# Kernel tuning notes

Hardware: AMD Instinct MI355X
Metric: run time of the kernel (lower is better)

Reference implementation:

```python
import jax, jax.numpy as jnp
import numpy as np

EPS = 1e-5
SEQ = 64

def ln(x, g, b):
    m = jnp.mean(x, axis=-1, keepdims=True)
    v = jnp.var(x, axis=-1, keepdims=True)
    return (x - m) / jnp.sqrt(v + EPS) * g + b

def gelu(x):
    return jax.nn.gelu(x, approximate=False)  # torch nn.GELU default = exact erf

def setup_inputs() -> dict:
    key = jax.random.key(0)
    ks = jax.random.split(key, 24)
    B, D = 512, 128
    DSGU = 4 * D          # 512
    DATTN = DSGU // 2     # 256
    DEXP = 4 * D          # 512 (tiny-attn expanded dim)
    TF = SEQ * D          # 8192
    H = int(1.1 * TF)     # 9011
    w = lambda k, s: jax.random.normal(k, s, dtype=jnp.float32) * 0.02
    return {
        "x": jax.random.normal(ks[0], (B, SEQ, D), dtype=jnp.float32),
        # TinyAttentionBlock
        "qkv_ln_g": jnp.ones((D,), jnp.float32), "qkv_ln_b": jnp.zeros((D,), jnp.float32),
        "qkv_w": w(ks[1], (D, 3 * DEXP)), "qkv_b": jnp.zeros((3 * DEXP,), jnp.float32),
        "attn_proj_w": w(ks[2], (DEXP, DATTN)), "attn_proj_b": jnp.zeros((DATTN,), jnp.float32),
        "attn_ln_g": jnp.ones((DATTN,), jnp.float32), "attn_ln_b": jnp.zeros((DATTN,), jnp.float32),
        "rel_bias": w(ks[3], (2 * SEQ - 1,)),
        "scale": jnp.asarray(1.0 / np.sqrt(D), jnp.float32),
        # SGU proj_in / proj_spatial / proj_out
        "pin_ln_g": jnp.ones((D,), jnp.float32), "pin_ln_b": jnp.zeros((D,), jnp.float32),
        "pin_w": w(ks[4], (D, DSGU)), "pin_b": jnp.zeros((DSGU,), jnp.float32),
        "sp_ln_g": jnp.ones((SEQ,), jnp.float32), "sp_ln_b": jnp.zeros((SEQ,), jnp.float32),
        "sp_w": w(ks[5], (SEQ, SEQ)), "sp_b": jnp.ones((SEQ,), jnp.float32),  # bias init 1.0 per source
        "pout_ln_g": jnp.ones((DATTN,), jnp.float32), "pout_ln_b": jnp.zeros((DATTN,), jnp.float32),
        "pout_w": w(ks[6], (DATTN, D)), "pout_b": jnp.zeros((D,), jnp.float32),
        # ResidualBlock MLP
        "mlp_ln_g": jnp.ones((TF,), jnp.float32), "mlp_ln_b": jnp.zeros((TF,), jnp.float32),
        "mlp_w1": w(ks[7], (TF, H)), "mlp_b1": jnp.zeros((H,), jnp.float32),
        "mlp_w2": w(ks[8], (H, TF)), "mlp_b2": jnp.zeros((TF,), jnp.float32),
    }

def reference(x, qkv_ln_g, qkv_ln_b, qkv_w, qkv_b, attn_proj_w, attn_proj_b,
              attn_ln_g, attn_ln_b, rel_bias, scale,
              pin_ln_g, pin_ln_b, pin_w, pin_b, sp_ln_g, sp_ln_b, sp_w, sp_b,
              pout_ln_g, pout_ln_b, pout_w, pout_b,
              mlp_ln_g, mlp_ln_b, mlp_w1, mlp_b1, mlp_w2, mlp_b2):
    B = x.shape[0]
    # --- TinyAttentionBlock ---
    h = ln(x, qkv_ln_g, qkv_ln_b) @ qkv_w + qkv_b          # [B,64,3*512]
    q, k, v = jnp.split(h, 3, axis=-1)                      # each [B,64,512]
    idx = jnp.arange(SEQ)
    rel = idx[None, :] - idx[:, None] + (SEQ - 1)           # [64,64] in [0,126]
    bias = rel_bias[rel]                                    # [64,64]
    attn = jnp.einsum('bnd,bmd->bnm', q, k) + bias
    attn = jax.nn.softmax(attn, axis=-1) * scale            # post-softmax scale (as in source)
    av = jnp.einsum('bnm,bmd->bnd', attn, v)                # [B,64,512]
    a = ln(av @ attn_proj_w + attn_proj_b, attn_ln_g, attn_ln_b)  # [B,64,256]
    # --- SpatialGatingUnit ---
    h2 = gelu(ln(x, pin_ln_g, pin_ln_b) @ pin_w + pin_b)    # [B,64,512]
    u, vv = jnp.split(h2, 2, axis=-1)                        # [B,64,256] each
    vt = jnp.swapaxes(vv, 1, 2)                              # [B,256,64]
    vt = gelu(ln(vt, sp_ln_g, sp_ln_b) @ sp_w + sp_b)        # spatial proj over seq dim
    vv = jnp.swapaxes(vt, 1, 2)                              # [B,64,256]
    out = u * (vv + a)
    out = ln(out, pout_ln_g, pout_ln_b) @ pout_w + pout_b    # [B,64,128]
    x = x + out
    # --- ResidualBlock MLP on flattened board ---
    xf = x.reshape(B, -1)                                    # [B,8192]
    h3 = gelu(ln(xf, mlp_ln_g, mlp_ln_b) @ mlp_w1 + mlp_b1)  # [B,9011]
    xf = xf + (h3 @ mlp_w2 + mlp_b2)
    return xf.reshape(B, SEQ, -1)
```

## Files before the change

### kernel.cpp

```cpp
#include <hip/hip_runtime.h>
#include <hip/hip_bf16.h>
#include <math.h>

typedef float f32x4 __attribute__((ext_vector_type(4)));
typedef float f32x2 __attribute__((ext_vector_type(2)));
typedef short s16x8 __attribute__((ext_vector_type(8)));
typedef short s16x4 __attribute__((ext_vector_type(4)));
typedef int   i32x4 __attribute__((ext_vector_type(4)));

__device__ __forceinline__ short f2bf(float f) {
  __hip_bfloat16 h = __float2bfloat16(f);
  return __builtin_bit_cast(short, h);
}
__device__ __forceinline__ float bf2f(short s) {
  __hip_bfloat16 h = __builtin_bit_cast(__hip_bfloat16, s);
  return __bfloat162float(h);
}
__device__ __forceinline__ float gelu_f(float x) {
  return 0.5f * x * (1.f + erff(x * 0.70710678118654752440f));
}
__device__ __forceinline__ float waveSum(float v) {
  #pragma unroll
  for (int d = 32; d; d >>= 1) v += __shfl_xor(v, d);
  return v;
}
__device__ __forceinline__ void softBarrier() {
  asm volatile("s_waitcnt lgkmcnt(0)" ::: "memory");
  __builtin_amdgcn_s_barrier();
  asm volatile("" ::: "memory");
}

__global__ __launch_bounds__(256) void ln_dual_k(
    const float* __restrict__ x,
    const float* __restrict__ qg, const float* __restrict__ qb,
    const float* __restrict__ pg, const float* __restrict__ pb,
    short* __restrict__ lnq, short* __restrict__ lnp)
{
  int w = threadIdx.x >> 6, lane = threadIdx.x & 63;
  size_t row = (size_t)blockIdx.x * 4 + w;
  f32x2 v = reinterpret_cast<const f32x2*>(x + row * 128)[lane];
  float s  = v[0] + v[1];
  float sq = v[0]*v[0] + v[1]*v[1];
  s = waveSum(s); sq = waveSum(sq);
  float m = s * (1.f/128.f);
  float rstd = rsqrtf(sq * (1.f/128.f) - m*m + 1e-5f);
  int c = lane * 2;
  float a0 = (v[0]-m)*rstd, a1 = (v[1]-m)*rstd;
  unsigned q0 = (unsigned short)f2bf(a0*qg[c] + qb[c]);
  unsigned q1 = (unsigned short)f2bf(a1*qg[c+1] + qb[c+1]);
  unsigned p0 = (unsigned short)f2bf(a0*pg[c] + pb[c]);
  unsigned p1 = (unsigned short)f2bf(a1*pg[c+1] + pb[c+1]);
  ((unsigned*)lnq)[row*64 + lane] = q0 | (q1 << 16);
  ((unsigned*)lnp)[row*64 + lane] = p0 | (p1 << 16);
}

__global__ __launch_bounds__(256) void ln256_k(
    const float* __restrict__ in,
    const float* __restrict__ g, const float* __restrict__ bb,
    float* __restrict__ out)
{
  int w = threadIdx.x >> 6, lane = threadIdx.x & 63;
  size_t row = (size_t)blockIdx.x * 4 + w;
  f32x4 v = reinterpret_cast<const f32x4*>(in + row * 256)[lane];
  float s  = v[0]+v[1]+v[2]+v[3];
  float sq = v[0]*v[0]+v[1]*v[1]+v[2]*v[2]+v[3]*v[3];
  s = waveSum(s); sq = waveSum(sq);
  float m = s * (1.f/256.f);
  float rstd = rsqrtf(sq * (1.f/256.f) - m*m + 1e-5f);
  f32x4 g4 = reinterpret_cast<const f32x4*>(g)[lane];
  f32x4 b4 = reinterpret_cast<const f32x4*>(bb)[lane];
  f32x4 o;
  #pragma unroll
  for (int k = 0; k < 4; ++k) o[k] = (v[k]-m)*rstd*g4[k] + b4[k];
  reinterpret_cast<f32x4*>(out + row * 256)[lane] = o;
}

__global__ __launch_bounds__(256) void ln8192_k(
    const float* __restrict__ x1,
    const float* __restrict__ g, const float* __restrict__ bb,
    short* __restrict__ lnxp)
{
  __shared__ float red[8];
  int t = threadIdx.x, w = t >> 6, lane = t & 63;
  int b = blockIdx.x;
  const f32x4* xr = reinterpret_cast<const f32x4*>(x1 + (size_t)b * 8192);
  f32x4 vals[8];
  float s = 0.f, sq = 0.f;
  #pragma unroll
  for (int i = 0; i < 8; ++i) {
    f32x4 v = xr[t + i*256];
    vals[i] = v;
    s  += v[0]+v[1]+v[2]+v[3];
    sq += v[0]*v[0]+v[1]*v[1]+v[2]*v[2]+v[3]*v[3];
  }
  s = waveSum(s); sq = waveSum(sq);
  if (lane == 0) { red[w] = s; red[4+w] = sq; }
  __syncthreads();
  s  = red[0]+red[1]+red[2]+red[3];
  sq = red[4]+red[5]+red[6]+red[7];
  float m = s * (1.f/8192.f);
  float rstd = rsqrtf(sq * (1.f/8192.f) - m*m + 1e-5f);
  #pragma unroll
  for (int i = 0; i < 8; ++i) {
    int idx = (t + i*256) * 4;
    f32x4 g4 = reinterpret_cast<const f32x4*>(g)[t + i*256];
    f32x4 b4 = reinterpret_cast<const f32x4*>(bb)[t + i*256];
    s16x4 o;
    #pragma unroll
    for (int k = 0; k < 4; ++k) o[k] = f2bf((vals[i][k]-m)*rstd*g4[k] + b4[k]);
    size_t paddr = ((size_t)(idx >> 6) * 512 + b) * 64 + (idx & 63);
    *reinterpret_cast<s16x4*>(&lnxp[paddr]) = o;
  }
}

template<int BM, int BN, int WM, int WN, int EPI>
__global__ __launch_bounds__(256) void gemm_k(
    const short* __restrict__ A, const float* __restrict__ Bw,
    const float* __restrict__ bias, const float* __restrict__ res,
    void* __restrict__ O0, void* __restrict__ O1,
    int M, int N, int K, int Nreal, int Kreal)
{
  constexpr int BK = 64;
  __shared__ __align__(16) short As[BM][BK + 8];
  __shared__ __align__(16) short Bs[BN][BK + 8];
  const int t = threadIdx.x;
  const int lane = t & 63;
  const int w = t >> 6;
  const int wm = w / WN, wn = w % WN;
  const int ln15 = lane & 15, hi = lane >> 4;
  const int m0 = blockIdx.y * BM;
  const int n0 = blockIdx.x * BN;

  f32x4 acc[4][4] = {};

  for (int k0 = 0; k0 < K; k0 += BK) {
    #pragma unroll
    for (int i = 0; i < (BM*BK)/(256*8); ++i) {
      int e = (i*256 + t) * 8;
      int r = e / BK, c = e % BK;
      *reinterpret_cast<i32x4*>(&As[r][c]) =
          *reinterpret_cast<const i32x4*>(&A[(size_t)(m0 + r) * K + k0 + c]);
    }
    #pragma unroll
    for (int i = 0; i < (BK*BN)/256; ++i) {
      int idx = i*256 + t;
      int n = idx % BN, k = idx / BN;
      int gk = k0 + k, gn = n0 + n;
      float v = (gk < Kreal && gn < Nreal) ? Bw[(size_t)gk * Nreal + gn] : 0.f;
      Bs[n][k] = f2bf(v);
    }
    __syncthreads();
    #pragma unroll
    for (int kk = 0; kk < BK; kk += 32) {
      s16x8 af[4], bfr[4];
      #pragma unroll
      for (int fm = 0; fm < 4; ++fm)
        af[fm] = *reinterpret_cast<const s16x8*>(&As[wm*64 + fm*16 + ln15][kk + hi*8]);
      #pragma unroll
      for (int fn = 0; fn < 4; ++fn)
        bfr[fn] = *reinterpret_cast<const s16x8*>(&Bs[wn*64 + fn*16 + ln15][kk + hi*8]);
      #pragma unroll
      for (int fm = 0; fm < 4; ++fm)
        #pragma unroll
        for (int fn = 0; fn < 4; ++fn)
          acc[fm][fn] = __builtin_amdgcn_mfma_f32_16x16x32_bf16(
              af[fm], bfr[fn], acc[fm][fn], 0, 0, 0);
    }
    __syncthreads();
  }

  #pragma unroll
  for (int fm = 0; fm < 4; ++fm) {
    #pragma unroll
    for (int fn = 0; fn < 4; ++fn) {
      #pragma unroll
      for (int j = 0; j < 4; ++j) {
        int row = m0 + wm*64 + fm*16 + hi*4 + j;
        int col = n0 + wn*64 + fn*16 + ln15;
        float v = acc[fm][fn][j];
        if constexpr (EPI == 0) {
          v += bias[col];
          ((short*)O0)[(size_t)row * N + col] = f2bf(v);
        } else if constexpr (EPI == 1) {
          v += bias[col];
          ((float*)O0)[(size_t)row * N + col] = v;
        } else if constexpr (EPI == 2) {
          v = gelu_f(v + bias[col]);
          if (col < 256) ((float*)O0)[(size_t)row * 256 + col] = v;
          else ((short*)O1)[(size_t)row * 256 + (col - 256)] = f2bf(v);
        } else {
          v += bias[col] + res[(size_t)row * N + col];
          ((float*)O0)[(size_t)row * N + col] = v;
        }
      }
    }
  }
}

__global__ __launch_bounds__(512, 2) void gemm_splitk9(
    const short* __restrict__ Ap, const float* __restrict__ Bw,
    float* __restrict__ part,
    int N, int K, int Kreal, int ldb, int kchunk, int ntiles)
{
  __shared__ __align__(16) short Bs[2][128 * 64];
  const int t = threadIdx.x, lane = t & 63, w = t >> 6;
  const int ln15 = lane & 15, hi = lane >> 4;
  const int nt = blockIdx.x % ntiles, z = blockIdx.x / ntiles;
  const int n0 = nt * 128;
  const int kbeg = z * kchunk;
  const int kend = (kbeg + kchunk < K) ? (kbeg + kchunk) : K;
  const int nsteps = (kend - kbeg) >> 6;

  const int bn = t & 127;
  const int bg0 = (t >> 7) * 2;
  const bool bok = (n0 + bn) < ldb;
  const int bsw = bn & 7;

  float br[16];
  auto loadB = [&](int k0) {
    const float* bp = Bw + (size_t)(k0 + bg0 * 8) * ldb + n0 + bn;
    #pragma unroll
    for (int m = 0; m < 16; ++m) {
      int gk = k0 + bg0 * 8 + m;
      br[m] = (bok && gk < Kreal) ? bp[(size_t)m * ldb] : 0.f;
    }
  };
  auto writeB = [&](int buf) {
    s16x8 v0, v1;
    #pragma unroll
    for (int m = 0; m < 8; ++m) { v0[m] = f2bf(br[m]); v1[m] = f2bf(br[8 + m]); }
    short* dst = &Bs[buf][bn * 64];
    *reinterpret_cast<s16x8*>(dst + ((bg0    ) ^ bsw) * 8) = v0;
    *reinterpret_cast<s16x8*>(dst + ((bg0 + 1) ^ bsw) * 8) = v1;
  };

  f32x4 acc[4][8] = {};

  loadB(kbeg);
  writeB(0);
  if (nsteps > 1) loadB(kbeg + 64);
  softBarrier();

  for (int s = 0; s < nsteps; ++s) {
    const int k0 = kbeg + s * 64;
    const short* atile = Ap + (size_t)(k0 >> 6) * 512 * 64;
    s16x8 af[8];
    #pragma unroll
    for (int kk = 0; kk < 2; ++kk)
      #pragma unroll
      for (int fm = 0; fm < 4; ++fm) {
        int row = w * 64 + fm * 16 + ln15;
        af[kk * 4 + fm] = *reinterpret_cast<const s16x8*>(
            &atile[row * 64 + (kk * 4 + hi) * 8]);
      }
    if (s + 1 < nsteps) writeB((s + 1) & 1);
    if (s + 2 < nsteps) loadB(kbeg + (s + 2) * 64);

    const short* bsrc = &Bs[s & 1][0];
    #pragma unroll
    for (int kk = 0; kk < 2; ++kk) {
      const int g = kk * 4 + hi;
      #pragma unroll
      for (int fn = 0; fn < 8; ++fn) {
        int row = fn * 16 + ln15;
        s16x8 bv = *reinterpret_cast<const s16x8*>(
            &bsrc[row * 64 + ((g ^ (row & 7)) * 8)]);
        #pragma unroll
        for (int fm = 0; fm < 4; ++fm)
          acc[fm][fn] = __builtin_amdgcn_mfma_f32_16x16x32_bf16(
              af[kk * 4 + fm], bv, acc[fm][fn], 0, 0, 0);
      }
    }
    softBarrier();
  }

  #pragma unroll
  for (int fm = 0; fm < 4; ++fm)
    #pragma unroll
    for (int fn = 0; fn < 8; ++fn)
      #pragma unroll
      for (int j = 0; j < 4; ++j) {
        int row = w * 64 + fm * 16 + hi * 4 + j;
        int col = n0 + fn * 16 + ln15;
        part[((size_t)z * 512 + row) * N + col] = acc[fm][fn][j];
      }
}

__global__ __launch_bounds__(256) void reduce_mlp1_k(
    const float* __restrict__ part, const float* __restrict__ bias,
    short* __restrict__ h3p, int N, int Nreal, int M, int ks)
{
  int col4 = (blockIdx.x * 256 + threadIdx.x) * 4;
  int row = blockIdx.y;
  if (col4 >= N) return;
  size_t base = (size_t)row * N + col4;
  size_t stride = (size_t)M * N;
  f32x4 s = *reinterpret_cast<const f32x4*>(part + base);
  for (int k = 1; k < ks; ++k)
    s += *reinterpret_cast<const f32x4*>(part + base + (size_t)k * stride);
  s16x4 o;
  #pragma unroll
  for (int j = 0; j < 4; ++j) {
    int c = col4 + j;
    float v = 0.f;
    if (c < Nreal) v = gelu_f(s[j] + bias[c]);
    o[j] = f2bf(v);
  }
  size_t paddr = ((size_t)(col4 >> 6) * 512 + row) * 64 + (col4 & 63);
  *reinterpret_cast<s16x4*>(&h3p[paddr]) = o;
}

__global__ __launch_bounds__(256) void reduce_mlp2_k(
    const float* __restrict__ part, const float* __restrict__ bias,
    const float* __restrict__ x1, float* __restrict__ out, int N, int M, int ks)
{
  int col4 = (blockIdx.x * 256 + threadIdx.x) * 4;
  int row = blockIdx.y;
  size_t base = (size_t)row * N + col4;
  size_t stride = (size_t)M * N;
  f32x4 s = *reinterpret_cast<const f32x4*>(part + base);
  for (int k = 1; k < ks; ++k)
    s += *reinterpret_cast<const f32x4*>(part + base + (size_t)k * stride);
  f32x4 b4 = *reinterpret_cast<const f32x4*>(bias + col4);
  f32x4 r4 = *reinterpret_cast<const f32x4*>(x1 + base);
  #pragma unroll
  for (int j = 0; j < 4; ++j) s[j] += b4[j] + r4[j];
  *reinterpret_cast<f32x4*>(out + base) = s;
}

__global__ __launch_bounds__(256) void attn_k(
    const short* __restrict__ qkv, const float* __restrict__ relb,
    const float* __restrict__ scale_p, short* __restrict__ av)
{
  __shared__ __align__(16) short qlds[64][136];
  __shared__ __align__(16) short klds[64][136];
  __shared__ __align__(16) short plds[64][72];
  __shared__ __align__(16) short vlds[128][72];
  __shared__ float rb[127];
  int t = threadIdx.x, lane = t & 63, w = t >> 6;
  int ln15 = lane & 15, hi = lane >> 4;
  int b = blockIdx.x;
  if (t < 127) rb[t] = relb[t];

  f32x4 sacc[4] = {};
  for (int kc = 0; kc < 4; ++kc) {
    #pragma unroll
    for (int i = 0; i < 4; ++i) {
      int e = (i*256 + t) * 8;
      int r = e >> 7, c = e & 127;
      size_t base = (size_t)(b*64 + r) * 1536 + kc*128 + c;
      *reinterpret_cast<i32x4*>(&qlds[r][c]) = *reinterpret_cast<const i32x4*>(&qkv[base]);
      *reinterpret_cast<i32x4*>(&klds[r][c]) = *reinterpret_cast<const i32x4*>(&qkv[base + 512]);
    }
    __syncthreads();
    #pragma unroll
    for (int kk = 0; kk < 128; kk += 32) {
      s16x8 aq = *reinterpret_cast<const s16x8*>(&qlds[16*w + ln15][kk + hi*8]);
      #pragma unroll
      for (int fn = 0; fn < 4; ++fn) {
        s16x8 bk = *reinterpret_cast<const s16x8*>(&klds[fn*16 + ln15][kk + hi*8]);
        sacc[fn] = __builtin_amdgcn_mfma_f32_16x16x32_bf16(aq, bk, sacc[fn], 0, 0, 0);
      }
    }
    __syncthreads();
  }

  float scale = scale_p[0];
  #pragma unroll
  for (int j = 0; j < 4; ++j) {
    int row = 16*w + hi*4 + j;
    float pv[4];
    float mx = -1e30f;
    #pragma unroll
    for (int fn = 0; fn < 4; ++fn) {
      int col = fn*16 + ln15;
      pv[fn] = sacc[fn][j] + rb[col - row + 63];
      mx = fmaxf(mx, pv[fn]);
    }
    #pragma unroll
    for (int d = 1; d < 16; d <<= 1) mx = fmaxf(mx, __shfl_xor(mx, d));
    float sum = 0.f;
    #pragma unroll
    for (int fn = 0; fn < 4; ++fn) { pv[fn] = __expf(pv[fn] - mx); sum += pv[fn]; }
    #pragma unroll
    for (int d = 1; d < 16; d <<= 1) sum += __shfl_xor(sum, d);
    float inv = scale / sum;
    #pragma unroll
    for (int fn = 0; fn < 4; ++fn) plds[row][fn*16 + ln15] = f2bf(pv[fn] * inv);
  }
  __syncthreads();

  for (int cc = 0; cc < 4; ++cc) {
    #pragma unroll
    for (int i = 0; i < 8; ++i) {
      int idx = i*256 + t;
      int s = idx >> 5, c4 = (idx & 31) * 4;
      s16x4 vw = *reinterpret_cast<const s16x4*>(
          &qkv[(size_t)(b*64 + s) * 1536 + 1024 + cc*128 + c4]);
      vlds[c4+0][s] = vw[0]; vlds[c4+1][s] = vw[1];
      vlds[c4+2][s] = vw[2]; vlds[c4+3][s] = vw[3];
    }
    __syncthreads();
    f32x4 pacc[8] = {};
    #pragma unroll
    for (int kk = 0; kk < 64; kk += 32) {
      s16x8 ap = *reinterpret_cast<const s16x8*>(&plds[16*w + ln15][kk + hi*8]);
      #pragma unroll
      for (int fn = 0; fn < 8; ++fn) {
        s16x8 bv = *reinterpret_cast<const s16x8*>(&vlds[fn*16 + ln15][kk + hi*8]);
        pacc[fn] = __builtin_amdgcn_mfma_f32_16x16x32_bf16(ap, bv, pacc[fn], 0, 0, 0);
      }
    }
    #pragma unroll
    for (int fn = 0; fn < 8; ++fn)
      #pragma unroll
      for (int j = 0; j < 4; ++j) {
        int row = b*64 + 16*w + hi*4 + j;
        int col = cc*128 + fn*16 + ln15;
        av[(size_t)row * 512 + col] = f2bf(pacc[fn][j]);
      }
    __syncthreads();
  }
}

__global__ __launch_bounds__(256) void gate_k(
    const float* __restrict__ u, const short* __restrict__ vbf,
    const float* __restrict__ a,
    const float* __restrict__ spg_g, const float* __restrict__ spg_b,
    const float* __restrict__ spw, const float* __restrict__ spb,
    const float* __restrict__ pog, const float* __restrict__ pob,
    short* __restrict__ outn)
{
  __shared__ __align__(16) short nvb[256][72];
  __shared__ __align__(16) short spwT[64][72];
  __shared__ float s_spg[64], s_spbl[64], s_spb[64];
  __shared__ float s_pog[256], s_pob[256];
  int t = threadIdx.x, lane = t & 63, w = t >> 6;
  int ln15 = lane & 15, hi = lane >> 4;
  int b = blockIdx.x;

  if (t < 64) { s_spg[t] = spg_g[t]; s_spbl[t] = spg_b[t]; s_spb[t] = spb[t]; }
  s_pog[t] = pog[t]; s_pob[t] = pob[t];
  #pragma unroll
  for (int i = 0; i < 16; ++i) {
    int idx = i*256 + t;
    int sr = idx >> 6, tc = idx & 63;
    spwT[tc][sr] = f2bf(spw[idx]);
  }

  float vvv[64];
  {
    int c = t;
    float s = 0.f, sq = 0.f;
    #pragma unroll
    for (int si = 0; si < 64; ++si) {
      float f = bf2f(vbf[(size_t)(b*64 + si) * 256 + c]);
      vvv[si] = f; s += f; sq += f*f;
    }
    float m = s * (1.f/64.f);
    float rstd = rsqrtf(sq * (1.f/64.f) - m*m + 1e-5f);
    __syncthreads();
    #pragma unroll
    for (int si = 0; si < 64; ++si)
      nvb[c][si] = f2bf((vvv[si]-m)*rstd*s_spg[si] + s_spbl[si]);
  }
  __syncthreads();

  f32x4 yacc[4][4] = {};
  #pragma unroll
  for (int kk = 0; kk < 64; kk += 32) {
    s16x8 af[4], bfr[4];
    #pragma unroll
    for (int fm = 0; fm < 4; ++fm)
      af[fm] = *reinterpret_cast<const s16x8*>(&nvb[64*w + fm*16 + ln15][kk + hi*8]);
    #pragma unroll
    for (int fn = 0; fn < 4; ++fn)
      bfr[fn] = *reinterpret_cast<const s16x8*>(&spwT[fn*16 + ln15][kk + hi*8]);
    #pragma unroll
    for (int fm = 0; fm < 4; ++fm)
      #pragma unroll
      for (int fn = 0; fn < 4; ++fn)
        yacc[fm][fn] = __builtin_amdgcn_mfma_f32_16x16x32_bf16(
            af[fm], bfr[fn], yacc[fm][fn], 0, 0, 0);
  }
  __syncthreads();

  short (*outl)[264] = reinterpret_cast<short(*)[264]>(&nvb[0][0]);
  #pragma unroll
  for (int fm = 0; fm < 4; ++fm) {
    #pragma unroll
    for (int fn = 0; fn < 4; ++fn) {
      int crow = 64*w + fm*16 + hi*4;
      int tcol = fn*16 + ln15;
      f32x4 u4 = *reinterpret_cast<const f32x4*>(&u[(size_t)(b*64 + tcol)*256 + crow]);
      f32x4 a4 = *reinterpret_cast<const f32x4*>(&a[(size_t)(b*64 + tcol)*256 + crow]);
      #pragma unroll
      for (int j = 0; j < 4; ++j) {
        float g = gelu_f(yacc[fm][fn][j] + s_spb[tcol]);
        float o = u4[j] * (g + a4[j]);
        outl[tcol][crow + j] = f2bf(o);
      }
    }
  }
  __syncthreads();

  #pragma unroll
  for (int ri = 0; ri < 16; ++ri) {
    int trow = w*16 + ri;
    int c = lane * 4;
    s16x4 raw = *reinterpret_cast<const s16x4*>(&outl[trow][c]);
    float f0 = bf2f(raw[0]), f1 = bf2f(raw[1]), f2 = bf2f(raw[2]), f3 = bf2f(raw[3]);
    float s  = f0+f1+f2+f3;
    float sq = f0*f0+f1*f1+f2*f2+f3*f3;
    s = waveSum(s); sq = waveSum(sq);
    float m = s * (1.f/256.f);
    float rstd = rsqrtf(sq * (1.f/256.f) - m*m + 1e-5f);
    s16x4 o;
    o[0] = f2bf((f0-m)*rstd*s_pog[c+0] + s_pob[c+0]);
    o[1] = f2bf((f1-m)*rstd*s_pog[c+1] + s_pob[c+1]);
    o[2] = f2bf((f2-m)*rstd*s_pog[c+2] + s_pob[c+2]);
    o[3] = f2bf((f3-m)*rstd*s_pog[c+3] + s_pob[c+3]);
    *reinterpret_cast<s16x4*>(&outn[(size_t)(b*64 + trow)*256 + c]) = o;
  }
}

extern "C" void kernel_launch(void* const* d_in, const int* in_sizes, int n_in,
                              void* d_out, int out_size, void* d_ws, size_t ws_size,
                              hipStream_t stream)
{
  const float* x          = (const float*)d_in[0];
  const float* qkv_ln_g   = (const float*)d_in[1];
  const float* qkv_ln_b   = (const float*)d_in[2];
  const float* qkv_w      = (const float*)d_in[3];
  const float* qkv_b      = (const float*)d_in[4];
  const float* attn_pw    = (const float*)d_in[5];
  const float* attn_pb    = (const float*)d_in[6];
  const float* attn_ln_g  = (const float*)d_in[7];
  const float* attn_ln_b  = (const float*)d_in[8];
  const float* rel_bias   = (const float*)d_in[9];
  const float* scale      = (const float*)d_in[10];
  const float* pin_ln_g   = (const float*)d_in[11];
  const float* pin_ln_b   = (const float*)d_in[12];
  const float* pin_w      = (const float*)d_in[13];
  const float* pin_b      = (const float*)d_in[14];
  const float* sp_ln_g    = (const float*)d_in[15];
  const float* sp_ln_b    = (const float*)d_in[16];
  const float* sp_w       = (const float*)d_in[17];
  const float* sp_b       = (const float*)d_in[18];
  const float* pout_ln_g  = (const float*)d_in[19];
  const float* pout_ln_b  = (const float*)d_in[20];
  const float* pout_w     = (const float*)d_in[21];
  const float* pout_b     = (const float*)d_in[22];
  const float* mlp_ln_g   = (const float*)d_in[23];
  const float* mlp_ln_b   = (const float*)d_in[24];
  const float* mlp_w1     = (const float*)d_in[25];
  const float* mlp_b1     = (const float*)d_in[26];
  const float* mlp_w2     = (const float*)d_in[27];
  const float* mlp_b2     = (const float*)d_in[28];

  char* ws = (char*)d_ws;
  short* lnq  = (short*)(ws + 0);
  short* lnp  = (short*)(ws + 8388608);
  short* qkvb = (short*)(ws + 16777216);
  short* avb  = (short*)(ws + 117440512);
  float* projb= (float*)(ws + 16777216);
  float* ab   = (float*)(ws + 50331648);
  float* ub   = (float*)(ws + 83886080);
  short* vbfb = (short*)(ws + 117440512);
  short* outnb= (short*)(ws + 134217728);
  float* x1b  = (float*)(ws + 0);
  short* lnxp = (short*)(ws + 150994944);
  short* h3p  = (short*)(ws + 159383552);
  float* partb= (float*)(ws + 16777216);

  ln_dual_k<<<8192, 256, 0, stream>>>(x, qkv_ln_g, qkv_ln_b, pin_ln_g, pin_ln_b, lnq, lnp);
  gemm_k<128,128,2,2,0><<<dim3(12,256), 256, 0, stream>>>(
      lnq, qkv_w, qkv_b, nullptr, qkvb, nullptr, 32768, 1536, 128, 1536, 128);
  attn_k<<<512, 256, 0, stream>>>(qkvb, rel_bias, scale, avb);
  gemm_k<128,128,2,2,1><<<dim3(2,256), 256, 0, stream>>>(
      avb, attn_pw, attn_pb, nullptr, projb, nullptr, 32768, 256, 512, 256, 512);
  ln256_k<<<8192, 256, 0, stream>>>(projb, attn_ln_g, attn_ln_b, ab);
  gemm_k<128,128,2,2,2><<<dim3(4,256), 256, 0, stream>>>(
      lnp, pin_w, pin_b, nullptr, ub, vbfb, 32768, 512, 128, 512, 128);
  gate_k<<<512, 256, 0, stream>>>(ub, vbfb, ab, sp_ln_g, sp_ln_b, sp_w, sp_b,
                                  pout_ln_g, pout_ln_b, outnb);
  gemm_k<128,128,2,2,3><<<dim3(1,256), 256, 0, stream>>>(
      outnb, pout_w, pout_b, x, x1b, nullptr, 32768, 128, 256, 128, 256);
  ln8192_k<<<512, 256, 0, stream>>>(x1b, mlp_ln_g, mlp_ln_b, lnxp);

  gemm_splitk9<<<213, 512, 0, stream>>>(
      lnxp, mlp_w1, partb, 9088, 8192, 8192,
      9011, 2752, 71);
  reduce_mlp1_k<<<dim3(9, 512), 256, 0, stream>>>(partb, mlp_b1, h3p, 9088, 9011, 512, 3);

  gemm_splitk9<<<256, 512, 0, stream>>>(
      h3p, mlp_w2, partb, 8192, 9088, 9011,
      8192, 2304, 64);
  reduce_mlp2_k<<<dim3(8, 512), 256, 0, stream>>>(partb, mlp_b2, x1b, (float*)d_out, 8192, 512, 4);
}
```

Measured before the change: 769.2 us.

## Fuse LayerNorm, QKV projection, attention, output projection and LN into one kernel

Replaces five launches (dual LN, QKV GEMM, attention, attn-proj GEMM, LN256) with a single per-batch kernel. Each block keeps LN output, Q/K/V chunks, the softmax probabilities and the attention output in LDS, so the large qkv, av and proj intermediates never go to global memory. In exchange, every block re-reads and converts the fp32 qkv_w and attn_proj_w weights into transposed bf16 LDS tiles. It also uses about 159 KB of LDS, which allows only one 4-wave block per CU and leaves little latency hiding.

```diff
diff --git a/kernel.cpp b/kernel.cpp
--- a/kernel.cpp
+++ b/kernel.cpp
@@ -30,86 +30,225 @@
   asm volatile("" ::: "memory");
 }
 
-__global__ __launch_bounds__(256) void ln_dual_k(
+__global__ __launch_bounds__(256) void fused_attn_k(
     const float* __restrict__ x,
-    const float* __restrict__ qg, const float* __restrict__ qb,
-    const float* __restrict__ pg, const float* __restrict__ pb,
-    short* __restrict__ lnq, short* __restrict__ lnp)
-{
-  int w = threadIdx.x >> 6, lane = threadIdx.x & 63;
-  size_t row = (size_t)blockIdx.x * 4 + w;
-  f32x2 v = reinterpret_cast<const f32x2*>(x + row * 128)[lane];
-  float s  = v[0] + v[1];
-  float sq = v[0]*v[0] + v[1]*v[1];
-  s = waveSum(s); sq = waveSum(sq);
-  float m = s * (1.f/128.f);
-  float rstd = rsqrtf(sq * (1.f/128.f) - m*m + 1e-5f);
-  int c = lane * 2;
-  float a0 = (v[0]-m)*rstd, a1 = (v[1]-m)*rstd;
-  unsigned q0 = (unsigned short)f2bf(a0*qg[c] + qb[c]);
-  unsigned q1 = (unsigned short)f2bf(a1*qg[c+1] + qb[c+1]);
-  unsigned p0 = (unsigned short)f2bf(a0*pg[c] + pb[c]);
-  unsigned p1 = (unsigned short)f2bf(a1*pg[c+1] + pb[c+1]);
-  ((unsigned*)lnq)[row*64 + lane] = q0 | (q1 << 16);
-  ((unsigned*)lnp)[row*64 + lane] = p0 | (p1 << 16);
-}
-
-__global__ __launch_bounds__(256) void ln256_k(
-    const float* __restrict__ in,
-    const float* __restrict__ g, const float* __restrict__ bb,
-    float* __restrict__ out)
-{
-  int w = threadIdx.x >> 6, lane = threadIdx.x & 63;
-  size_t row = (size_t)blockIdx.x * 4 + w;
-  f32x4 v = reinterpret_cast<const f32x4*>(in + row * 256)[lane];
-  float s  = v[0]+v[1]+v[2]+v[3];
-  float sq = v[0]*v[0]+v[1]*v[1]+v[2]*v[2]+v[3]*v[3];
-  s = waveSum(s); sq = waveSum(sq);
-  float m = s * (1.f/256.f);
-  float rstd = rsqrtf(sq * (1.f/256.f) - m*m + 1e-5f);
-  f32x4 g4 = reinterpret_cast<const f32x4*>(g)[lane];
-  f32x4 b4 = reinterpret_cast<const f32x4*>(bb)[lane];
-  f32x4 o;
-  #pragma unroll
-  for (int k = 0; k < 4; ++k) o[k] = (v[k]-m)*rstd*g4[k] + b4[k];
-  reinterpret_cast<f32x4*>(out + row * 256)[lane] = o;
-}
-
-__global__ __launch_bounds__(256) void ln8192_k(
-    const float* __restrict__ x1,
-    const float* __restrict__ g, const float* __restrict__ bb,
-    short* __restrict__ lnxp)
-{
-  __shared__ float red[8];
-  int t = threadIdx.x, w = t >> 6, lane = t & 63;
-  int b = blockIdx.x;
-  const f32x4* xr = reinterpret_cast<const f32x4*>(x1 + (size_t)b * 8192);
-  f32x4 vals[8];
-  float s = 0.f, sq = 0.f;
-  #pragma unroll
-  for (int i = 0; i < 8; ++i) {
-    f32x4 v = xr[t + i*256];
-    vals[i] = v;
-    s  += v[0]+v[1]+v[2]+v[3];
-    sq += v[0]*v[0]+v[1]*v[1]+v[2]*v[2]+v[3]*v[3];
-  }
-  s = waveSum(s); sq = waveSum(sq);
-  if (lane == 0) { red[w] = s; red[4+w] = sq; }
+    const float* __restrict__ qln_g, const float* __restrict__ qln_b,
+    const float* __restrict__ pln_g, const float* __restrict__ pln_b,
+    const float* __restrict__ qkv_w, const float* __restrict__ qkv_b,
+    const float* __restrict__ attn_pw, const float* __restrict__ attn_pb,
+    const float* __restrict__ aln_g, const float* __restrict__ aln_b,
+    const float* __restrict__ relb, const float* __restrict__ scale_p,
+    short* __restrict__ lnp, float* __restrict__ ab)
+{
+  __shared__ __align__(16) char arena[159232];
+  short (*lnq)[136]  = reinterpret_cast<short(*)[136]>(arena + 0);
+  short (*plds)[72]  = reinterpret_cast<short(*)[72]>(arena + 17408);
+  short (*vlds)[72]  = reinterpret_cast<short(*)[72]>(arena + 26624);
+  short (*avl)[136]  = reinterpret_cast<short(*)[136]>(arena + 26624);
+  short (*qlds)[136] = reinterpret_cast<short(*)[136]>(arena + 45056);
+  short (*klds)[136] = reinterpret_cast<short(*)[136]>(arena + 62464);
+  short (*pwT)[136]  = reinterpret_cast<short(*)[136]>(arena + 45056);
+  short (*wT)[136]   = reinterpret_cast<short(*)[136]>(arena + 114688);
+  float* rb    = reinterpret_cast<float*>(arena + 149504);
+  float* s_apb = reinterpret_cast<float*>(arena + 150016);
+  float* s_ag  = reinterpret_cast<float*>(arena + 151040);
+  float* s_ab2 = reinterpret_cast<float*>(arena + 152064);
+  float* sqb   = reinterpret_cast<float*>(arena + 153088);
+
+  const int t = threadIdx.x, lane = t & 63, w = t >> 6;
+  const int ln15 = lane & 15, hi = lane >> 4;
+  const int b = blockIdx.x;
+
+  if (t < 127) rb[t] = relb[t];
+  s_apb[t] = attn_pb[t]; s_ag[t] = aln_g[t]; s_ab2[t] = aln_b[t];
+  #pragma unroll
+  for (int i = 0; i < 6; ++i) sqb[i*256 + t] = qkv_b[i*256 + t];
+
+  {
+    int c = lane * 2;
+    float qg0 = qln_g[c], qg1 = qln_g[c+1], qb0 = qln_b[c], qb1 = qln_b[c+1];
+    float pg0 = pln_g[c], pg1 = pln_g[c+1], pb0 = pln_b[c], pb1 = pln_b[c+1];
+    for (int i = 0; i < 16; ++i) {
+      int r = w * 16 + i;
+      f32x2 v = *reinterpret_cast<const f32x2*>(&x[((size_t)b*64 + r)*128 + c]);
+      float s = v[0] + v[1], sq = v[0]*v[0] + v[1]*v[1];
+      s = waveSum(s); sq = waveSum(sq);
+      float m = s * (1.f/128.f);
+      float rstd = rsqrtf(sq*(1.f/128.f) - m*m + 1e-5f);
+      float a0 = (v[0]-m)*rstd, a1 = (v[1]-m)*rstd;
+      unsigned q0 = (unsigned short)f2bf(a0*qg0 + qb0);
+      unsigned q1 = (unsigned short)f2bf(a1*qg1 + qb1);
+      *reinterpret_cast<unsigned*>(&lnq[r][c]) = q0 | (q1 << 16);
+      unsigned p0 = (unsigned short)f2bf(a0*pg0 + pb0);
+      unsigned p1 = (unsigned short)f2bf(a1*pg1 + pb1);
+      ((unsigned*)lnp)[((size_t)b*64 + r)*64 + lane] = p0 | (p1 << 16);
+    }
+  }
   __syncthreads();
-  s  = red[0]+red[1]+red[2]+red[3];
-  sq = red[4]+red[5]+red[6]+red[7];
-  float m = s * (1.f/8192.f);
-  float rstd = rsqrtf(sq * (1.f/8192.f) - m*m + 1e-5f);
-  #pragma unroll
-  for (int i = 0; i < 8; ++i) {
-    int idx = (t + i*256) * 4;
-    f32x4 g4 = reinterpret_cast<const f32x4*>(g)[t + i*256];
-    f32x4 b4 = reinterpret_cast<const f32x4*>(bb)[t + i*256];
-    s16x4 o;
-    #pragma unroll
-    for (int k = 0; k < 4; ++k) o[k] = f2bf((vals[i][k]-m)*rstd*g4[k] + b4[k]);
-    size_t paddr = ((size_t)(idx >> 6) * 512 + b) * 64 + (idx & 63);
-    *reinterpret_cast<s16x4*>(&lnxp[paddr]) = o;
+
+  auto stageW = [&](int coff) {
+    #pragma unroll
+    for (int i = 0; i < 16; ++i) {
+      int e = i*256 + t;
+      int k = e >> 5, c4 = (e & 31) * 4;
+      f32x4 v = *reinterpret_cast<const f32x4*>(&qkv_w[(size_t)k*1536 + coff + c4]);
+      wT[c4+0][k] = f2bf(v[0]); wT[c4+1][k] = f2bf(v[1]);
+      wT[c4+2][k] = f2bf(v[2]); wT[c4+3][k] = f2bf(v[3]);
+    }
+  };
+  auto gemm8 = [&](f32x4 (&acc)[8]) {
+    #pragma unroll
+    for (int kk = 0; kk < 4; ++kk) {
+      s16x8 af = *reinterpret_cast<const s16x8*>(&lnq[w*16 + ln15][kk*32 + hi*8]);
+      #pragma unroll
+      for (int fn = 0; fn < 8; ++fn) {
+        s16x8 bf = *reinterpret_cast<const s16x8*>(&wT[fn*16 + ln15][kk*32 + hi*8]);
+        acc[fn] = __builtin_amdgcn_mfma_f32_16x16x32_bf16(af, bf, acc[fn], 0, 0, 0);
+      }
+    }
+  };
+
+  f32x4 sacc[4] = {};
+  for (int kc = 0; kc < 4; ++kc) {
+    __syncthreads();
+    stageW(kc * 128);
+    __syncthreads();
+    {
+      f32x4 qa[8] = {};
+      gemm8(qa);
+      #pragma unroll
+      for (int fn = 0; fn < 8; ++fn) {
+        float bias = sqb[kc*128 + fn*16 + ln15];
+        #pragma unroll
+        for (int j = 0; j < 4; ++j)
+          qlds[w*16 + hi*4 + j][fn*16 + ln15] = f2bf(qa[fn][j] + bias);
+      }
+    }
+    __syncthreads();
+    stageW(512 + kc * 128);
+    __syncthreads();
+    {
+      f32x4 ka[8] = {};
+      gemm8(ka);
+      #pragma unroll
+      for (int fn = 0; fn < 8; ++fn) {
+        float bias = sqb[512 + kc*128 + fn*16 + ln15];
+        #pragma unroll
+        for (int j = 0; j < 4; ++j)
+          klds[w*16 + hi*4 + j][fn*16 + ln15] = f2bf(ka[fn][j] + bias);
+      }
+    }
+    __syncthreads();
+    #pragma unroll
+    for (int kk = 0; kk < 4; ++kk) {
+      s16x8 aq = *reinterpret_cast<const s16x8*>(&qlds[16*w + ln15][kk*32 + hi*8]);
+      #pragma unroll
+      for (int fn = 0; fn < 4; ++fn) {
+        s16x8 bk = *reinterpret_cast<const s16x8*>(&klds[fn*16 + ln15][kk*32 + hi*8]);
+        sacc[fn] = __builtin_amdgcn_mfma_f32_16x16x32_bf16(aq, bk, sacc[fn], 0, 0, 0);
+      }
+    }
+  }
+
+  {
+    float scale = scale_p[0];
+    #pragma unroll
+    for (int j = 0; j < 4; ++j) {
+      int row = 16*w + hi*4 + j;
+      float pv[4];
+      float mx = -1e30f;
+      #pragma unroll
+      for (int fn = 0; fn < 4; ++fn) {
+        int col = fn*16 + ln15;
+        pv[fn] = sacc[fn][j] + rb[col - row + 63];
+        mx = fmaxf(mx, pv[fn]);
+      }
+      #pragma unroll
+      for (int d = 1; d < 16; d <<= 1) mx = fmaxf(mx, __shfl_xor(mx, d));
+      float sum = 0.f;
+      #pragma unroll
+      for (int fn = 0; fn < 4; ++fn) { pv[fn] = __expf(pv[fn] - mx); sum += pv[fn]; }
+      #pragma unroll
+      for (int d = 1; d < 16; d <<= 1) sum += __shfl_xor(sum, d);
+      float inv = scale / sum;
+      #pragma unroll
+      for (int fn = 0; fn < 4; ++fn) plds[row][fn*16 + ln15] = f2bf(pv[fn] * inv);
+    }
+  }
+  __syncthreads();
+
+  f32x4 pracc[16] = {};
+  for (int cc = 0; cc < 4; ++cc) {
+    __syncthreads();
+    stageW(1024 + cc * 128);
+    #pragma unroll
+    for (int i = 0; i < 32; ++i) {
+      int e = i*256 + t;
+      int k = e >> 6, c4 = (e & 63) * 4;
+      f32x4 v = *reinterpret_cast<const f32x4*>(&attn_pw[(size_t)(cc*128 + k)*256 + c4]);
+      pwT[c4+0][k] = f2bf(v[0]); pwT[c4+1][k] = f2bf(v[1]);
+      pwT[c4+2][k] = f2bf(v[2]); pwT[c4+3][k] = f2bf(v[3]);
+    }
+    __syncthreads();
+    {
+      f32x4 va[8] = {};
+      gemm8(va);
+      #pragma unroll
+      for (int fn = 0; fn < 8; ++fn) {
+        float bias = sqb[1024 + cc*128 + fn*16 + ln15];
+        #pragma unroll
+        for (int j = 0; j < 4; ++j)
+          vlds[fn*16 + ln15][w*16 + hi*4 + j] = f2bf(va[fn][j] + bias);
+      }
+    }
+    __syncthreads();
+    f32x4 pacc[8] = {};
+    #pragma unroll
+    for (int kk = 0; kk < 2; ++kk) {
+      s16x8 ap = *reinterpret_cast<const s16x8*>(&plds[16*w + ln15][kk*32 + hi*8]);
+      #pragma unroll
+      for (int fn = 0; fn < 8; ++fn) {
+        s16x8 bv = *reinterpret_cast<const s16x8*>(&vlds[fn*16 + ln15][kk*32 + hi*8]);
+        pacc[fn] = __builtin_amdgcn_mfma_f32_16x16x32_bf16(ap, bv, pacc[fn], 0, 0, 0);
+      }
+    }
+    __syncthreads();
+    #pragma unroll
+    for (int fn = 0; fn < 8; ++fn)
+      #pragma unroll
+      for (int j = 0; j < 4; ++j)
+        avl[w*16 + hi*4 + j][fn*16 + ln15] = f2bf(pacc[fn][j]);
+    __syncthreads();
+    #pragma unroll
+    for (int kk = 0; kk < 4; ++kk) {
+      s16x8 aa = *reinterpret_cast<const s16x8*>(&avl[16*w + ln15][kk*32 + hi*8]);
+      #pragma unroll
+      for (int fn = 0; fn < 16; ++fn) {
+        s16x8 pb = *reinterpret_cast<const s16x8*>(&pwT[fn*16 + ln15][kk*32 + hi*8]);
+        pracc[fn] = __builtin_amdgcn_mfma_f32_16x16x32_bf16(aa, pb, pracc[fn], 0, 0, 0);
+      }
+    }
+  }
+
+  #pragma unroll
+  for (int j = 0; j < 4; ++j) {
+    int row = 16*w + hi*4 + j;
+    float vv[16];
+    float s = 0.f, sq = 0.f;
+    #pragma unroll
+    for (int fn = 0; fn < 16; ++fn) {
+      vv[fn] = pracc[fn][j] + s_apb[fn*16 + ln15];
+      s += vv[fn]; sq += vv[fn]*vv[fn];
+    }
+    #pragma unroll
+    for (int d = 1; d < 16; d <<= 1) { s += __shfl_xor(s, d); sq += __shfl_xor(sq, d); }
+    float m = s * (1.f/256.f);
+    float rstd = rsqrtf(sq*(1.f/256.f) - m*m + 1e-5f);
+    #pragma unroll
+    for (int fn = 0; fn < 16; ++fn) {
+      int col = fn*16 + ln15;
+      ab[((size_t)b*64 + row)*256 + col] = (vv[fn]-m)*rstd*s_ag[col] + s_ab2[col];
+    }
   }
 }
 
@@ -178,13 +317,7 @@
         int row = m0 + wm*64 + fm*16 + hi*4 + j;
         int col = n0 + wn*64 + fn*16 + ln15;
         float v = acc[fm][fn][j];
-        if constexpr (EPI == 0) {
-          v += bias[col];
-          ((short*)O0)[(size_t)row * N + col] = f2bf(v);
-        } else if constexpr (EPI == 1) {
-          v += bias[col];
-          ((float*)O0)[(size_t)row * N + col] = v;
-        } else if constexpr (EPI == 2) {
+        if constexpr (EPI == 2) {
           v = gelu_f(v + bias[col]);
           if (col < 256) ((float*)O0)[(size_t)row * 256 + col] = v;
           else ((short*)O1)[(size_t)row * 256 + (col - 256)] = f2bf(v);
@@ -194,6 +327,44 @@
         }
       }
     }
+  }
+}
+
+__global__ __launch_bounds__(256) void ln8192_k(
+    const float* __restrict__ x1,
+    const float* __restrict__ g, const float* __restrict__ bb,
+    short* __restrict__ lnxp)
+{
+  __shared__ float red[8];
+  int t = threadIdx.x, w = t >> 6, lane = t & 63;
+  int b = blockIdx.x;
+  const f32x4* xr = reinterpret_cast<const f32x4*>(x1 + (size_t)b * 8192);
+  f32x4 vals[8];
+  float s = 0.f, sq = 0.f;
+  #pragma unroll
+  for (int i = 0; i < 8; ++i) {
+    f32x4 v = xr[t + i*256];
+    vals[i] = v;
+    s  += v[0]+v[1]+v[2]+v[3];
+    sq += v[0]*v[0]+v[1]*v[1]+v[2]*v[2]+v[3]*v[3];
+  }
+  s = waveSum(s); sq = waveSum(sq);
+  if (lane == 0) { red[w] = s; red[4+w] = sq; }
+  __syncthreads();
+  s  = red[0]+red[1]+red[2]+red[3];
+  sq = red[4]+red[5]+red[6]+red[7];
+  float m = s * (1.f/8192.f);
+  float rstd = rsqrtf(sq * (1.f/8192.f) - m*m + 1e-5f);
+  #pragma unroll
+  for (int i = 0; i < 8; ++i) {
+    int idx = (t + i*256) * 4;
+    f32x4 g4 = reinterpret_cast<const f32x4*>(g)[t + i*256];
+    f32x4 b4 = reinterpret_cast<const f32x4*>(bb)[t + i*256];
+    s16x4 o;
+    #pragma unroll
+    for (int k = 0; k < 4; ++k) o[k] = f2bf((vals[i][k]-m)*rstd*g4[k] + b4[k]);
+    size_t paddr = ((size_t)(idx >> 6) * 512 + b) * 64 + (idx & 63);
+    *reinterpret_cast<s16x4*>(&lnxp[paddr]) = o;
   }
 }
 
@@ -326,101 +497,6 @@
   #pragma unroll
   for (int j = 0; j < 4; ++j) s[j] += b4[j] + r4[j];
   *reinterpret_cast<f32x4*>(out + base) = s;
-}
-
-__global__ __launch_bounds__(256) void attn_k(
-    const short* __restrict__ qkv, const float* __restrict__ relb,
-    const float* __restrict__ scale_p, short* __restrict__ av)
-{
-  __shared__ __align__(16) short qlds[64][136];
-  __shared__ __align__(16) short klds[64][136];
-  __shared__ __align__(16) short plds[64][72];
-  __shared__ __align__(16) short vlds[128][72];
-  __shared__ float rb[127];
-  int t = threadIdx.x, lane = t & 63, w = t >> 6;
-  int ln15 = lane & 15, hi = lane >> 4;
-  int b = blockIdx.x;
-  if (t < 127) rb[t] = relb[t];
-
-  f32x4 sacc[4] = {};
-  for (int kc = 0; kc < 4; ++kc) {
-    #pragma unroll
-    for (int i = 0; i < 4; ++i) {
-      int e = (i*256 + t) * 8;
-      int r = e >> 7, c = e & 127;
-      size_t base = (size_t)(b*64 + r) * 1536 + kc*128 + c;
-      *reinterpret_cast<i32x4*>(&qlds[r][c]) = *reinterpret_cast<const i32x4*>(&qkv[base]);
-      *reinterpret_cast<i32x4*>(&klds[r][c]) = *reinterpret_cast<const i32x4*>(&qkv[base + 512]);
-    }
-    __syncthreads();
-    #pragma unroll
-    for (int kk = 0; kk < 128; kk += 32) {
-      s16x8 aq = *reinterpret_cast<const s16x8*>(&qlds[16*w + ln15][kk + hi*8]);
-      #pragma unroll
-      for (int fn = 0; fn < 4; ++fn) {
-        s16x8 bk = *reinterpret_cast<const s16x8*>(&klds[fn*16 + ln15][kk + hi*8]);
-        sacc[fn] = __builtin_amdgcn_mfma_f32_16x16x32_bf16(aq, bk, sacc[fn], 0, 0, 0);
-      }
-    }
-    __syncthreads();
-  }
-
-  float scale = scale_p[0];
-  #pragma unroll
-  for (int j = 0; j < 4; ++j) {
-    int row = 16*w + hi*4 + j;
-    float pv[4];
-    float mx = -1e30f;
-    #pragma unroll
-    for (int fn = 0; fn < 4; ++fn) {
-      int col = fn*16 + ln15;
-      pv[fn] = sacc[fn][j] + rb[col - row + 63];
-      mx = fmaxf(mx, pv[fn]);
-    }
-    #pragma unroll
-    for (int d = 1; d < 16; d <<= 1) mx = fmaxf(mx, __shfl_xor(mx, d));
-    float sum = 0.f;
-    #pragma unroll
-    for (int fn = 0; fn < 4; ++fn) { pv[fn] = __expf(pv[fn] - mx); sum += pv[fn]; }
-    #pragma unroll
-    for (int d = 1; d < 16; d <<= 1) sum += __shfl_xor(sum, d);
-    float inv = scale / sum;
-    #pragma unroll
-    for (int fn = 0; fn < 4; ++fn) plds[row][fn*16 + ln15] = f2bf(pv[fn] * inv);
-  }
-  __syncthreads();
-
-  for (int cc = 0; cc < 4; ++cc) {
-    #pragma unroll
-    for (int i = 0; i < 8; ++i) {
-      int idx = i*256 + t;
-      int s = idx >> 5, c4 = (idx & 31) * 4;
-      s16x4 vw = *reinterpret_cast<const s16x4*>(
-          &qkv[(size_t)(b*64 + s) * 1536 + 1024 + cc*128 + c4]);
-      vlds[c4+0][s] = vw[0]; vlds[c4+1][s] = vw[1];
-      vlds[c4+2][s] = vw[2]; vlds[c4+3][s] = vw[3];
-    }
-    __syncthreads();
-    f32x4 pacc[8] = {};
-    #pragma unroll
-    for (int kk = 0; kk < 64; kk += 32) {
-      s16x8 ap = *reinterpret_cast<const s16x8*>(&plds[16*w + ln15][kk + hi*8]);
-      #pragma unroll
-      for (int fn = 0; fn < 8; ++fn) {
-        s16x8 bv = *reinterpret_cast<const s16x8*>(&vlds[fn*16 + ln15][kk + hi*8]);
-        pacc[fn] = __builtin_amdgcn_mfma_f32_16x16x32_bf16(ap, bv, pacc[fn], 0, 0, 0);
-      }
-    }
-    #pragma unroll
-    for (int fn = 0; fn < 8; ++fn)
-      #pragma unroll
-      for (int j = 0; j < 4; ++j) {
-        int row = b*64 + 16*w + hi*4 + j;
-        int col = cc*128 + fn*16 + ln15;
-        av[(size_t)row * 512 + col] = f2bf(pacc[fn][j]);
-      }
-    __syncthreads();
-  }
 }
 
 __global__ __launch_bounds__(256) void gate_k(
@@ -559,27 +635,19 @@
   const float* mlp_b2     = (const float*)d_in[28];
 
   char* ws = (char*)d_ws;
-  short* lnq  = (short*)(ws + 0);
-  short* lnp  = (short*)(ws + 8388608);
-  short* qkvb = (short*)(ws + 16777216);
-  short* avb  = (short*)(ws + 117440512);
-  float* projb= (float*)(ws + 16777216);
-  float* ab   = (float*)(ws + 50331648);
-  float* ub   = (float*)(ws + 83886080);
-  short* vbfb = (short*)(ws + 117440512);
-  short* outnb= (short*)(ws + 134217728);
-  float* x1b  = (float*)(ws + 0);
-  short* lnxp = (short*)(ws + 150994944);
-  short* h3p  = (short*)(ws + 159383552);
-  float* partb= (float*)(ws + 16777216);
-
-  ln_dual_k<<<8192, 256, 0, stream>>>(x, qkv_ln_g, qkv_ln_b, pin_ln_g, pin_ln_b, lnq, lnp);
-  gemm_k<128,128,2,2,0><<<dim3(12,256), 256, 0, stream>>>(
-      lnq, qkv_w, qkv_b, nullptr, qkvb, nullptr, 32768, 1536, 128, 1536, 128);
-  attn_k<<<512, 256, 0, stream>>>(qkvb, rel_bias, scale, avb);
-  gemm_k<128,128,2,2,1><<<dim3(2,256), 256, 0, stream>>>(
-      avb, attn_pw, attn_pb, nullptr, projb, nullptr, 32768, 256, 512, 256, 512);
-  ln256_k<<<8192, 256, 0, stream>>>(projb, attn_ln_g, attn_ln_b, ab);
+  short* lnp   = (short*)(ws + 0);
+  float* x1b   = (float*)(ws + 0);
+  float* ab    = (float*)(ws + 16777216);
+  float* ub    = (float*)(ws + 50331648);
+  short* vbfb  = (short*)(ws + 83886080);
+  short* outnb = (short*)(ws + 100663296);
+  short* lnxp  = (short*)(ws + 150994944);
+  short* h3p   = (short*)(ws + 159383552);
+  float* partb = (float*)(ws + 16777216);
+
+  fused_attn_k<<<512, 256, 0, stream>>>(
+      x, qkv_ln_g, qkv_ln_b, pin_ln_g, pin_ln_b, qkv_w, qkv_b,
+      attn_pw, attn_pb, attn_ln_g, attn_ln_b, rel_bias, scale, lnp, ab);
   gemm_k<128,128,2,2,2><<<dim3(4,256), 256, 0, stream>>>(
       lnp, pin_w, pin_b, nullptr, ub, vbfb, 32768, 512, 128, 512, 128);
   gate_k<<<512, 256, 0, stream>>>(ub, vbfb, ab, sp_ln_g, sp_ln_b, sp_w, sp_b,
```

Measured after the change: 765.0 us. Within noise of the previous version (-0.5%).
